# Performance work log

Hardware: AMD Instinct MI355X
Metric: run time of the kernel (lower is better)

The kernel has to match this reference:

```python
import jax, jax.numpy as jnp
import numpy as np

B, L = 4096, 2048
TAU = 0.85        # DivLoss tau (augmented=True)
MARGIN = 0.0005   # RerankLoss margin
RW = 0.5          # rerank_weight
CW = 0.5          # classi_weight


def setup_inputs() -> dict:
    key = jax.random.key(0)
    k1, k2, k3, k4 = jax.random.split(key, 4)
    # cut_y: per-row probability distribution over L cut positions (softmax output)
    cut_y = jax.nn.softmax(jax.random.normal(k1, (B, L)), axis=1)[..., None]
    # pred_y: sigmoid-like probabilities in (0,1) for BCE
    pred_y = jax.random.uniform(k2, (B, L, 1)) * 0.98 + 0.01
    rerank_y = jax.random.normal(k3, (B, L, 1))
    labels = jax.random.randint(k4, (B, L), 0, 2).astype(jnp.float32)
    return {"pred_y": pred_y, "rerank_y": rerank_y, "cut_y": cut_y, "labels": labels}


def _kl_batchmean(target, log_input):
    # torch.nn.KLDivLoss(reduction='batchmean'): sum(target*(log target - log_input)) / B
    term = jnp.where(target > 0, target * (jnp.log(jnp.where(target > 0, target, 1.0)) - log_input), 0.0)
    return jnp.sum(term) / target.shape[0]


def reference(pred_y, rerank_y, cut_y, labels):
    Bn, Ln = labels.shape
    # ---- DivLoss (metric='f1', div_type='js', augmented=True) ----
    # Vectorized replacement of the per-element double loop:
    # f1 at cut k: p = c/k, r = c/T -> 2*c/(k+T) where c = #relevant in top-k
    c = jnp.cumsum(labels, axis=1)                     # [B,L] prefix relevant counts
    T = c[:, -1:]                                      # [B,1] total relevant per row
    k = jnp.arange(1, Ln + 1, dtype=labels.dtype)      # cut positions 1..L
    r = 2.0 * c / (k[None, :] + T)                     # f1 reward per cut position
    q = jax.nn.softmax(r / TAU, axis=1)                # q = exp(r/tau)/sum
    p = cut_y[..., 0]                                  # output.squeeze()
    log_mean = jnp.log((p + q) * 0.5)
    cutloss = 0.5 * (_kl_batchmean(q, log_mean) + _kl_batchmean(p, log_mean))
    # ---- RerankLoss (hinge on mean pos vs mean neg scores) ----
    s = rerank_y[..., 0]
    pos = (labels == 1.0)
    neg = (labels == 0.0)
    pos_mean = jnp.sum(jnp.where(pos, s, 0.0)) / jnp.sum(pos)
    neg_mean = jnp.sum(jnp.where(neg, s, 0.0)) / jnp.sum(neg)
    rerankloss = jnp.maximum(0.0, neg_mean - pos_mean + MARGIN) * RW
    # ---- BCELoss ----
    pp = pred_y[..., 0]
    bce = -jnp.mean(labels * jnp.log(pp) + (1.0 - labels) * jnp.log(1.0 - pp)) * CW
    return cutloss + rerankloss + bce
```

## Files before the change

kernel.cpp:

```cpp
#include <hip/hip_runtime.h>

namespace {
constexpr int Bn = 4096;
constexpr int Ln = 2048;
constexpr float TAU = 0.85f;
constexpr float MARGIN = 0.0005f;
constexpr float RW = 0.5f;
constexpr float CW = 0.5f;

constexpr int THREADS = 256;
constexpr int EPT = Ln / THREADS;
static_assert(EPT == 8, "layout assumption");

__global__ __launch_bounds__(THREADS) void mt_row_kernel(
    const float* __restrict__ pred,
    const float* __restrict__ rerank,
    const float* __restrict__ cut,
    const float* __restrict__ labels,
    float* __restrict__ part)
{
  const int row  = blockIdx.x;
  const int tid  = threadIdx.x;
  const int lane = tid & 63;
  const int wid  = tid >> 6;
  const size_t base = (size_t)row * Ln + (size_t)tid * EPT;

  __shared__ float wtot[4];
  __shared__ float smax[4];
  __shared__ float ssumS[4];
  __shared__ float sacc[4][4];

  float4 la = *reinterpret_cast<const float4*>(labels + base);
  float4 lb = *reinterpret_cast<const float4*>(labels + base + 4);
  float lab[8] = {la.x, la.y, la.z, la.w, lb.x, lb.y, lb.z, lb.w};
  float pref[8];
  float run = 0.f;
  #pragma unroll
  for (int j = 0; j < 8; ++j) { run += lab[j]; pref[j] = run; }
  const float own = run;

  float sc = own;
  #pragma unroll
  for (int off = 1; off < 64; off <<= 1) {
    float n = __shfl_up(sc, off, 64);
    if (lane >= off) sc += n;
  }
  if (lane == 63) wtot[wid] = sc;
  __syncthreads();
  float woff = 0.f;
  #pragma unroll
  for (int w = 0; w < 4; ++w) if (w < wid) woff += wtot[w];
  const float T = wtot[0] + wtot[1] + wtot[2] + wtot[3];
  const float excl = woff + sc - own;

  float e[8];
  float zmax = -3.4e38f;
  const float kbase = (float)(tid * EPT);
  #pragma unroll
  for (int j = 0; j < 8; ++j) {
    float c = excl + pref[j];
    float k = kbase + (float)(j + 1);
    float z = (2.f * c / (k + T)) * (1.f / TAU);
    e[j] = z;
    zmax = fmaxf(zmax, z);
  }
  #pragma unroll
  for (int off = 32; off > 0; off >>= 1) zmax = fmaxf(zmax, __shfl_xor(zmax, off, 64));
  if (lane == 0) smax[wid] = zmax;
  __syncthreads();
  zmax = fmaxf(fmaxf(smax[0], smax[1]), fmaxf(smax[2], smax[3]));

  float esum = 0.f;
  #pragma unroll
  for (int j = 0; j < 8; ++j) { e[j] = __expf(e[j] - zmax); esum += e[j]; }
  #pragma unroll
  for (int off = 32; off > 0; off >>= 1) esum += __shfl_xor(esum, off, 64);
  if (lane == 0) ssumS[wid] = esum;
  __syncthreads();
  esum = ssumS[0] + ssumS[1] + ssumS[2] + ssumS[3];
  const float inv = 1.f / esum;

  float4 pa = *reinterpret_cast<const float4*>(cut + base);
  float4 pb = *reinterpret_cast<const float4*>(cut + base + 4);
  float p[8] = {pa.x, pa.y, pa.z, pa.w, pb.x, pb.y, pb.z, pb.w};
  float kl = 0.f;
  #pragma unroll
  for (int j = 0; j < 8; ++j) {
    float q  = e[j] * inv;
    float lm = __logf((p[j] + q) * 0.5f);
    kl += q * (__logf(q) - lm) + p[j] * (__logf(p[j]) - lm);
  }

  float4 sa = *reinterpret_cast<const float4*>(rerank + base);
  float4 sb = *reinterpret_cast<const float4*>(rerank + base + 4);
  float sv[8] = {sa.x, sa.y, sa.z, sa.w, sb.x, sb.y, sb.z, sb.w};
  float s_all = 0.f, s_pos = 0.f;
  #pragma unroll
  for (int j = 0; j < 8; ++j) { s_all += sv[j]; s_pos += sv[j] * lab[j]; }

  float4 ya = *reinterpret_cast<const float4*>(pred + base);
  float4 yb = *reinterpret_cast<const float4*>(pred + base + 4);
  float y[8] = {ya.x, ya.y, ya.z, ya.w, yb.x, yb.y, yb.z, yb.w};
  float bce = 0.f;
  #pragma unroll
  for (int j = 0; j < 8; ++j) {
    float x = (lab[j] == 1.f) ? y[j] : (1.f - y[j]);
    bce += __logf(x);
  }

  #pragma unroll
  for (int off = 32; off > 0; off >>= 1) {
    kl    += __shfl_xor(kl,    off, 64);
    s_all += __shfl_xor(s_all, off, 64);
    s_pos += __shfl_xor(s_pos, off, 64);
    bce   += __shfl_xor(bce,   off, 64);
  }
  if (lane == 0) { sacc[wid][0] = kl; sacc[wid][1] = s_all; sacc[wid][2] = s_pos; sacc[wid][3] = bce; }
  __syncthreads();
  if (tid == 0) {
    part[0 * Bn + row] = sacc[0][0] + sacc[1][0] + sacc[2][0] + sacc[3][0];
    part[1 * Bn + row] = sacc[0][1] + sacc[1][1] + sacc[2][1] + sacc[3][1];
    part[2 * Bn + row] = sacc[0][2] + sacc[1][2] + sacc[2][2] + sacc[3][2];
    part[3 * Bn + row] = sacc[0][3] + sacc[1][3] + sacc[2][3] + sacc[3][3];
    part[4 * Bn + row] = T;
  }
}

__global__ __launch_bounds__(256) void mt_final_kernel(
    const float* __restrict__ part, float* __restrict__ out)
{
  const int tid  = threadIdx.x;
  const int lane = tid & 63;
  const int wid  = tid >> 6;
  double kl = 0, sv = 0, sp = 0, bc = 0, tt = 0;
  for (int r = tid; r < Bn; r += 256) {
    kl += (double)part[0 * Bn + r];
    sv += (double)part[1 * Bn + r];
    sp += (double)part[2 * Bn + r];
    bc += (double)part[3 * Bn + r];
    tt += (double)part[4 * Bn + r];
  }
  #pragma unroll
  for (int off = 32; off > 0; off >>= 1) {
    kl += __shfl_xor(kl, off, 64);
    sv += __shfl_xor(sv, off, 64);
    sp += __shfl_xor(sp, off, 64);
    bc += __shfl_xor(bc, off, 64);
    tt += __shfl_xor(tt, off, 64);
  }
  __shared__ double sh[4][5];
  if (lane == 0) { sh[wid][0] = kl; sh[wid][1] = sv; sh[wid][2] = sp; sh[wid][3] = bc; sh[wid][4] = tt; }
  __syncthreads();
  if (tid == 0) {
    kl = sh[0][0] + sh[1][0] + sh[2][0] + sh[3][0];
    sv = sh[0][1] + sh[1][1] + sh[2][1] + sh[3][1];
    sp = sh[0][2] + sh[1][2] + sh[2][2] + sh[3][2];
    bc = sh[0][3] + sh[1][3] + sh[2][3] + sh[3][3];
    tt = sh[0][4] + sh[1][4] + sh[2][4] + sh[3][4];
    const double total = (double)Bn * (double)Ln;
    const double posc = tt, negc = total - tt;
    double rer = (sv - sp) / negc - sp / posc + (double)MARGIN;
    if (rer < 0.0) rer = 0.0;
    rer *= (double)RW;
    const double cutl = 0.5 * kl / (double)Bn;
    const double bcel = -(bc / total) * (double)CW;
    out[0] = (float)(cutl + rer + bcel);
  }
}
}

extern "C" void kernel_launch(void* const* d_in, const int* in_sizes, int n_in,
                              void* d_out, int out_size, void* d_ws, size_t ws_size,
                              hipStream_t stream) {
  const float* pred   = (const float*)d_in[0];
  const float* rerank = (const float*)d_in[1];
  const float* cut    = (const float*)d_in[2];
  const float* labels = (const float*)d_in[3];
  float* part = (float*)d_ws;
  mt_row_kernel<<<Bn, THREADS, 0, stream>>>(pred, rerank, cut, labels, part);
  mt_final_kernel<<<1, 256, 0, stream>>>(part, (float*)d_out);
}
```

Before: 152.7 us.

## Drop softmax max pass, fold q·log q analytically, and issue all loads up front

Removes the row-max reduction and one barrier by exponentiating z directly, which is safe because z lies in [0, 2/tau]. The per-element q*log q term is replaced by the closed form sum(e*z)/esum - log(esum), computed once per row. All four input loads are issued at the start so their latency overlaps the scan and softmax work. The p*log p term and the BCE and rerank sums are also computed early. In exchange the kernel relies on the bounded range of z, changes floating-point rounding slightly, and holds more values in registers.

```diff
diff --git a/kernel.cpp b/kernel.cpp
--- a/kernel.cpp
+++ b/kernel.cpp
@@ -26,19 +26,38 @@
   const size_t base = (size_t)row * Ln + (size_t)tid * EPT;
 
   __shared__ float wtot[4];
-  __shared__ float smax[4];
-  __shared__ float ssumS[4];
+  __shared__ float smid[4][2];
   __shared__ float sacc[4][4];
 
-  float4 la = *reinterpret_cast<const float4*>(labels + base);
-  float4 lb = *reinterpret_cast<const float4*>(labels + base + 4);
-  float lab[8] = {la.x, la.y, la.z, la.w, lb.x, lb.y, lb.z, lb.w};
+  const float4 la = *reinterpret_cast<const float4*>(labels + base);
+  const float4 lb = *reinterpret_cast<const float4*>(labels + base + 4);
+  const float4 ya = *reinterpret_cast<const float4*>(pred   + base);
+  const float4 yb = *reinterpret_cast<const float4*>(pred   + base + 4);
+  const float4 sa = *reinterpret_cast<const float4*>(rerank + base);
+  const float4 sb = *reinterpret_cast<const float4*>(rerank + base + 4);
+  const float4 pa = *reinterpret_cast<const float4*>(cut    + base);
+  const float4 pb = *reinterpret_cast<const float4*>(cut    + base + 4);
+
+  const float lab[8] = {la.x, la.y, la.z, la.w, lb.x, lb.y, lb.z, lb.w};
+  const float y[8]   = {ya.x, ya.y, ya.z, ya.w, yb.x, yb.y, yb.z, yb.w};
+  const float sv[8]  = {sa.x, sa.y, sa.z, sa.w, sb.x, sb.y, sb.z, sb.w};
+  const float p[8]   = {pa.x, pa.y, pa.z, pa.w, pb.x, pb.y, pb.z, pb.w};
+
+  float bce = 0.f, s_all = 0.f, s_pos = 0.f, plp = 0.f;
+  #pragma unroll
+  for (int j = 0; j < 8; ++j) {
+    const float x = (lab[j] == 1.f) ? y[j] : (1.f - y[j]);
+    bce   += __logf(x);
+    s_all += sv[j];
+    s_pos += sv[j] * lab[j];
+    plp   += p[j] * __logf(p[j]);
+  }
+
   float pref[8];
   float run = 0.f;
   #pragma unroll
   for (int j = 0; j < 8; ++j) { run += lab[j]; pref[j] = run; }
   const float own = run;
-
   float sc = own;
   #pragma unroll
   for (int off = 1; off < 64; off <<= 1) {
@@ -54,58 +73,35 @@
   const float excl = woff + sc - own;
 
   float e[8];
-  float zmax = -3.4e38f;
+  float esum = 0.f, t1 = 0.f;
   const float kbase = (float)(tid * EPT);
   #pragma unroll
   for (int j = 0; j < 8; ++j) {
-    float c = excl + pref[j];
-    float k = kbase + (float)(j + 1);
-    float z = (2.f * c / (k + T)) * (1.f / TAU);
-    e[j] = z;
-    zmax = fmaxf(zmax, z);
+    const float c = excl + pref[j];
+    const float k = kbase + (float)(j + 1);
+    const float z = __fdividef(2.f * c, (k + T) * TAU);
+    const float ev = __expf(z);
+    e[j] = ev;
+    esum += ev;
+    t1   += ev * z;
   }
   #pragma unroll
-  for (int off = 32; off > 0; off >>= 1) zmax = fmaxf(zmax, __shfl_xor(zmax, off, 64));
-  if (lane == 0) smax[wid] = zmax;
+  for (int off = 32; off > 0; off >>= 1) {
+    esum += __shfl_xor(esum, off, 64);
+    t1   += __shfl_xor(t1,   off, 64);
+  }
+  if (lane == 0) { smid[wid][0] = esum; smid[wid][1] = t1; }
   __syncthreads();
-  zmax = fmaxf(fmaxf(smax[0], smax[1]), fmaxf(smax[2], smax[3]));
-
-  float esum = 0.f;
-  #pragma unroll
-  for (int j = 0; j < 8; ++j) { e[j] = __expf(e[j] - zmax); esum += e[j]; }
-  #pragma unroll
-  for (int off = 32; off > 0; off >>= 1) esum += __shfl_xor(esum, off, 64);
-  if (lane == 0) ssumS[wid] = esum;
-  __syncthreads();
-  esum = ssumS[0] + ssumS[1] + ssumS[2] + ssumS[3];
+  esum = smid[0][0] + smid[1][0] + smid[2][0] + smid[3][0];
+  t1   = smid[0][1] + smid[1][1] + smid[2][1] + smid[3][1];
   const float inv = 1.f / esum;
 
-  float4 pa = *reinterpret_cast<const float4*>(cut + base);
-  float4 pb = *reinterpret_cast<const float4*>(cut + base + 4);
-  float p[8] = {pa.x, pa.y, pa.z, pa.w, pb.x, pb.y, pb.z, pb.w};
-  float kl = 0.f;
+  float kl = plp;
   #pragma unroll
   for (int j = 0; j < 8; ++j) {
-    float q  = e[j] * inv;
-    float lm = __logf((p[j] + q) * 0.5f);
-    kl += q * (__logf(q) - lm) + p[j] * (__logf(p[j]) - lm);
-  }
-
-  float4 sa = *reinterpret_cast<const float4*>(rerank + base);
-  float4 sb = *reinterpret_cast<const float4*>(rerank + base + 4);
-  float sv[8] = {sa.x, sa.y, sa.z, sa.w, sb.x, sb.y, sb.z, sb.w};
-  float s_all = 0.f, s_pos = 0.f;
-  #pragma unroll
-  for (int j = 0; j < 8; ++j) { s_all += sv[j]; s_pos += sv[j] * lab[j]; }
-
-  float4 ya = *reinterpret_cast<const float4*>(pred + base);
-  float4 yb = *reinterpret_cast<const float4*>(pred + base + 4);
-  float y[8] = {ya.x, ya.y, ya.z, ya.w, yb.x, yb.y, yb.z, yb.w};
-  float bce = 0.f;
-  #pragma unroll
-  for (int j = 0; j < 8; ++j) {
-    float x = (lab[j] == 1.f) ? y[j] : (1.f - y[j]);
-    bce += __logf(x);
+    const float q  = e[j] * inv;
+    const float lm = __logf((p[j] + q) * 0.5f);
+    kl -= (p[j] + q) * lm;
   }
 
   #pragma unroll
@@ -118,7 +114,9 @@
   if (lane == 0) { sacc[wid][0] = kl; sacc[wid][1] = s_all; sacc[wid][2] = s_pos; sacc[wid][3] = bce; }
   __syncthreads();
   if (tid == 0) {
-    part[0 * Bn + row] = sacc[0][0] + sacc[1][0] + sacc[2][0] + sacc[3][0];
+    const float klrow = sacc[0][0] + sacc[1][0] + sacc[2][0] + sacc[3][0]
+                      + t1 * inv - __logf(esum);
+    part[0 * Bn + row] = klrow;
     part[1 * Bn + row] = sacc[0][1] + sacc[1][1] + sacc[2][1] + sacc[3][1];
     part[2 * Bn + row] = sacc[0][2] + sacc[1][2] + sacc[2][2] + sacc[3][2];
     part[3 * Bn + row] = sacc[0][3] + sacc[1][3] + sacc[2][3] + sacc[3][3];
```

New measurement: 155.8 us. 2.1% more time.
